# Kernel tuning notes

Hardware: AMD Instinct MI355X
Metric: run time of the kernel (lower is better)

The kernel has to match this reference:

```python
import jax, jax.numpy as jnp
import numpy as np

NUM_SCALE_LAYERS = [16, 8, 8]


def _pool2s1(x):
    # MaxPool1d(kernel=2, stride=1): length L -> L-1
    return jnp.maximum(x[..., :-1], x[..., 1:])


def _pool3s2(x):
    # MaxPool1d(kernel=3, stride=2): length L -> (L-3)//2 + 1
    L = x.shape[-1]
    n = (L - 3) // 2 + 1
    return jnp.maximum(jnp.maximum(x[..., 0:2 * n:2], x[..., 1:2 * n + 1:2]),
                       x[..., 2:2 * n + 2:2])


def setup_inputs() -> dict:
    key = jax.random.key(0)
    x = jax.random.normal(key, (32, 512, 64), dtype=jnp.float32)
    return {"x": x}


def reference(x):
    B, H, N = x.shape
    ori = N  # scale 0 has stride-1 first layer, so ori_num_clips == N
    map_h = jnp.zeros((B, H, ori, ori), dtype=x.dtype)
    map_mask = jnp.zeros((B, 1, ori, ori), dtype=x.dtype)
    acum = 0
    stride = 1
    for scale_idx, num_layer in enumerate(NUM_SCALE_LAYERS):
        for i in range(num_layer):
            if i == 0:
                if scale_idx > 0:
                    x = _pool3s2(x)
                    stride *= 2
                # scale 0 first layer is MaxPool1d(1,1) == identity, stride*=1
            else:
                x = _pool2s1(x)
            # diagonal scatter directly into the original-resolution map
            s_idx = np.arange(0, ori - acum - i * stride, stride)
            e_idx = s_idx + acum + i * stride
            map_h = map_h.at[:, :, s_idx, e_idx].set(x)
            map_mask = map_mask.at[:, :, s_idx, e_idx].set(jnp.ones((), x.dtype))
        acum += stride * (num_layer + 1)
    return map_h, map_mask
```

## Files before the change

### kernel.cpp

```cpp
#include <hip/hip_runtime.h>
#include <hip/hip_bf16.h>


#define BB 32
#define HH 512
#define NN 64

__device__ __forceinline__ unsigned long long active_mask_for_e(int e) {
    unsigned long long m;
    if (e >= 15) m = 0xFFFFull << (e - 15);
    else         m = 0xFFFFull >> (15 - e);
    if ((e & 1) && e >= 17) {
        int a = e - 31; if (a < 0) a = 0;
        int b = e - 17;
        unsigned long long r = (~0ull >> (63 - b)) & (~0ull << a);
        m |= r & 0x5555555555555555ull;
    }
    if (((e & 3) == 3) && e >= 35) {
        int b = e - 35;
        unsigned long long r = (~0ull >> (63 - b));
        m |= r & 0x1111111111111111ull;
    }
    return m;
}

__global__ __launch_bounds__(256) void sppool_map_kernel(
        const float* __restrict__ x, float* __restrict__ map_h) {
    __shared__ float xs[16][65];
    const int tid  = threadIdx.x;
    const int lrow = tid >> 4;
    const int e0   = (tid & 15) << 2;
    const size_t rowbase = (size_t)blockIdx.x * 16;

    const float* xin = x + rowbase * NN;
    for (int i = tid; i < 16 * NN; i += 256)
        xs[i >> 6][i & 63] = xin[i];
    __syncthreads();

    const float* xr = xs[lrow];
    const unsigned long long am0 = active_mask_for_e(e0 + 0);
    const unsigned long long am1 = active_mask_for_e(e0 + 1);
    const unsigned long long am2 = active_mask_for_e(e0 + 2);
    const unsigned long long am3 = active_mask_for_e(e0 + 3);

    float m0 = -INFINITY, m1 = -INFINITY, m2 = -INFINITY, m3 = -INFINITY;
    float* out = map_h + (rowbase + lrow) * (NN * NN) + e0;

    #pragma unroll 8
    for (int s = 63; s >= 0; --s) {
        const float xv = xr[s];
        m0 = fmaxf(m0, (s <= e0 + 0) ? xv : -INFINITY);
        m1 = fmaxf(m1, (s <= e0 + 1) ? xv : -INFINITY);
        m2 = fmaxf(m2, (s <= e0 + 2) ? xv : -INFINITY);
        m3 = fmaxf(m3, (s <= e0 + 3) ? xv : -INFINITY);
        float4 v;
        v.x = ((am0 >> s) & 1ull) ? m0 : 0.0f;
        v.y = ((am1 >> s) & 1ull) ? m1 : 0.0f;
        v.z = ((am2 >> s) & 1ull) ? m2 : 0.0f;
        v.w = ((am3 >> s) & 1ull) ? m3 : 0.0f;
        *(float4*)(out + (size_t)s * NN) = v;
    }
}

__global__ __launch_bounds__(256) void sppool_mask_kernel(
        float* __restrict__ mask_out) {
    const int idx = blockIdx.x * 256 + threadIdx.x;
    if (idx >= BB * NN * NN / 4) return;
    const int e0 = (idx & 15) << 2;
    const int s  = (idx >> 4) & 63;
    float4 v;
    v.x = ((active_mask_for_e(e0 + 0) >> s) & 1ull) ? 1.0f : 0.0f;
    v.y = ((active_mask_for_e(e0 + 1) >> s) & 1ull) ? 1.0f : 0.0f;
    v.z = ((active_mask_for_e(e0 + 2) >> s) & 1ull) ? 1.0f : 0.0f;
    v.w = ((active_mask_for_e(e0 + 3) >> s) & 1ull) ? 1.0f : 0.0f;
    ((float4*)mask_out)[idx] = v;
}

extern "C" void kernel_launch(void* const* d_in, const int* in_sizes, int n_in,
                              void* d_out, int out_size, void* d_ws, size_t ws_size,
                              hipStream_t stream) {
    const float* x = (const float*)d_in[0];
    float* map_h   = (float*)d_out;
    float* map_mask = (float*)d_out + (size_t)BB * HH * NN * NN;

    sppool_map_kernel<<<BB * HH / 16, 256, 0, stream>>>(x, map_h);
    sppool_mask_kernel<<<(BB * NN * NN / 4 + 255) / 256, 256, 0, stream>>>(map_mask);
}
```

Baseline: 254.7 us.

## Fuse map and mask kernels; use sparse-table range max with coalesced writes

Replaces the per-thread sequential running max with a shared-memory sparse table (log-doubling max levels), so each output element is a constant-time two-lookup range max. Each block now handles 4 rows and writes each row's 64x64 output as contiguous float4 stores across the whole block, instead of 16 rows with strided per-thread column writes. The mask kernel is folded into the same launch as extra blocks, removing a second launch. It adds several __syncthreads to build the table and uses 4x more blocks. The kernel mostly writes about 1 GB of output, so it is likely bandwidth-bound.

New measurement: 260.6 us. +2.3%, slower.

```diff
diff --git a/kernel.cpp b/kernel.cpp
--- a/kernel.cpp
+++ b/kernel.cpp
@@ -2,9 +2,10 @@
 #include <hip/hip_bf16.h>
 
 
-#define BB 32
-#define HH 512
 #define NN 64
+#define MAPROWS (32 * 512)
+#define MAPBLOCKS (MAPROWS / 4)
+#define MASKBLOCKS 32
 
 __device__ __forceinline__ unsigned long long active_mask_for_e(int e) {
     unsigned long long m;
@@ -24,65 +25,80 @@
     return m;
 }
 
-__global__ __launch_bounds__(256) void sppool_map_kernel(
-        const float* __restrict__ x, float* __restrict__ map_h) {
-    __shared__ float xs[16][65];
-    const int tid  = threadIdx.x;
-    const int lrow = tid >> 4;
-    const int e0   = (tid & 15) << 2;
-    const size_t rowbase = (size_t)blockIdx.x * 16;
+__device__ __forceinline__ float range_max(const float (*Tr)[65], int s, int e,
+                                           unsigned long long am) {
+    int dp1 = e - s + 1;
+    if (dp1 < 1) dp1 = 1;
+    const int k = 31 - __clz(dp1);
+    const float va = Tr[k][s];
+    const float vb = Tr[k][e + 1 - (1 << k)];
+    const float v = fmaxf(va, vb);
+    return ((am >> s) & 1ull) ? v : 0.0f;
+}
 
-    const float* xin = x + rowbase * NN;
-    for (int i = tid; i < 16 * NN; i += 256)
-        xs[i >> 6][i & 63] = xin[i];
-    __syncthreads();
+__global__ __launch_bounds__(256) void sppool_fused_kernel(
+        const float* __restrict__ x, float* __restrict__ out) {
+    const int tid = threadIdx.x;
+    const int bid = blockIdx.x;
+    const int e0 = (tid & 15) << 2;
 
-    const float* xr = xs[lrow];
     const unsigned long long am0 = active_mask_for_e(e0 + 0);
     const unsigned long long am1 = active_mask_for_e(e0 + 1);
     const unsigned long long am2 = active_mask_for_e(e0 + 2);
     const unsigned long long am3 = active_mask_for_e(e0 + 3);
 
-    float m0 = -INFINITY, m1 = -INFINITY, m2 = -INFINITY, m3 = -INFINITY;
-    float* out = map_h + (rowbase + lrow) * (NN * NN) + e0;
+    if (bid < MAPBLOCKS) {
+        __shared__ float T[4][7][65];
+        const int r = tid >> 6;
+        const int t = tid & 63;
+        const size_t row0 = (size_t)bid * 4;
 
-    #pragma unroll 8
-    for (int s = 63; s >= 0; --s) {
-        const float xv = xr[s];
-        m0 = fmaxf(m0, (s <= e0 + 0) ? xv : -INFINITY);
-        m1 = fmaxf(m1, (s <= e0 + 1) ? xv : -INFINITY);
-        m2 = fmaxf(m2, (s <= e0 + 2) ? xv : -INFINITY);
-        m3 = fmaxf(m3, (s <= e0 + 3) ? xv : -INFINITY);
-        float4 v;
-        v.x = ((am0 >> s) & 1ull) ? m0 : 0.0f;
-        v.y = ((am1 >> s) & 1ull) ? m1 : 0.0f;
-        v.z = ((am2 >> s) & 1ull) ? m2 : 0.0f;
-        v.w = ((am3 >> s) & 1ull) ? m3 : 0.0f;
-        *(float4*)(out + (size_t)s * NN) = v;
+        T[r][0][t] = x[row0 * NN + tid];
+        __syncthreads();
+        #pragma unroll
+        for (int k = 1; k <= 6; ++k) {
+            const int half = 1 << (k - 1);
+            const int t2 = (t + half < 63) ? (t + half) : 63;
+            const float a = T[r][k - 1][t];
+            const float b = T[r][k - 1][t2];
+            T[r][k][t] = fmaxf(a, b);
+            __syncthreads();
+        }
+
+        float4* ochunk = (float4*)(out + row0 * (size_t)(NN * NN));
+        #pragma unroll 4
+        for (int i = 0; i < 16; ++i) {
+            const int rr = i >> 2;
+            const int s = ((i & 3) << 4) + (tid >> 4);
+            const float (*Tr)[65] = T[rr];
+            float4 v;
+            v.x = range_max(Tr, s, e0 + 0, am0);
+            v.y = range_max(Tr, s, e0 + 1, am1);
+            v.z = range_max(Tr, s, e0 + 2, am2);
+            v.w = range_max(Tr, s, e0 + 3, am3);
+            ochunk[i * 256 + tid] = v;
+        }
+    } else {
+        const int mb = bid - MAPBLOCKS;
+        float4* mchunk = (float4*)(out + (size_t)MAPROWS * NN * NN
+                                       + (size_t)mb * NN * NN);
+        #pragma unroll
+        for (int i = 0; i < 4; ++i) {
+            const int s = (i << 4) + (tid >> 4);
+            float4 v;
+            v.x = ((am0 >> s) & 1ull) ? 1.0f : 0.0f;
+            v.y = ((am1 >> s) & 1ull) ? 1.0f : 0.0f;
+            v.z = ((am2 >> s) & 1ull) ? 1.0f : 0.0f;
+            v.w = ((am3 >> s) & 1ull) ? 1.0f : 0.0f;
+            mchunk[i * 256 + tid] = v;
+        }
     }
-}
-
-__global__ __launch_bounds__(256) void sppool_mask_kernel(
-        float* __restrict__ mask_out) {
-    const int idx = blockIdx.x * 256 + threadIdx.x;
-    if (idx >= BB * NN * NN / 4) return;
-    const int e0 = (idx & 15) << 2;
-    const int s  = (idx >> 4) & 63;
-    float4 v;
-    v.x = ((active_mask_for_e(e0 + 0) >> s) & 1ull) ? 1.0f : 0.0f;
-    v.y = ((active_mask_for_e(e0 + 1) >> s) & 1ull) ? 1.0f : 0.0f;
-    v.z = ((active_mask_for_e(e0 + 2) >> s) & 1ull) ? 1.0f : 0.0f;
-    v.w = ((active_mask_for_e(e0 + 3) >> s) & 1ull) ? 1.0f : 0.0f;
-    ((float4*)mask_out)[idx] = v;
 }
 
 extern "C" void kernel_launch(void* const* d_in, const int* in_sizes, int n_in,
                               void* d_out, int out_size, void* d_ws, size_t ws_size,
                               hipStream_t stream) {
     const float* x = (const float*)d_in[0];
-    float* map_h   = (float*)d_out;
-    float* map_mask = (float*)d_out + (size_t)BB * HH * NN * NN;
-
-    sppool_map_kernel<<<BB * HH / 16, 256, 0, stream>>>(x, map_h);
-    sppool_mask_kernel<<<(BB * NN * NN / 4 + 255) / 256, 256, 0, stream>>>(map_mask);
+    float* out = (float*)d_out;
+    sppool_fused_kernel<<<MAPBLOCKS + MASKBLOCKS, 256, 0, stream>>>(x, out);
 }
```
